# Kernel optimization log

Measured on AMD Instinct MI355X. Metric: run time of the kernel, lower is better.

## Reference

```python
import jax, jax.numpy as jnp
import numpy as np

N = 100000   # nodes
E = 1600000  # edges (avg degree 16)
IN_F = 256
OUT_F = 128


def setup_inputs() -> dict:
    key = jax.random.key(0)
    k1, k2, k3, k4, k5, k6 = jax.random.split(key, 6)
    std = 1.0 / (OUT_F ** 0.5)
    return {
        "x": jax.random.normal(k1, (N, IN_F), dtype=jnp.float32),
        "weight": jax.random.uniform(k2, (IN_F, OUT_F), dtype=jnp.float32, minval=-std, maxval=std),
        "bias": jax.random.uniform(k3, (OUT_F,), dtype=jnp.float32, minval=-std, maxval=std),
        "edge_weight": jax.random.uniform(k4, (E,), dtype=jnp.float32),
        "row": jax.random.randint(k5, (E,), 0, N, dtype=jnp.int32),
        "col": jax.random.randint(k6, (E,), 0, N, dtype=jnp.int32),
    }


def reference(x, weight, bias, edge_weight, row, col):
    # support = x @ W : dense GEMM [N, in] x [in, out]
    support = jnp.matmul(x, weight)
    # spmm(adj, support): gather source-node rows, scale by edge value,
    # scatter-add into destination rows (COO SpMM).
    msgs = support[col] * edge_weight[:, None]          # [E, out]
    aggregated = jax.ops.segment_sum(msgs, row, num_segments=N)  # [N, out]
    return aggregated + bias
```

## Files before the change

### kernel.cpp

```cpp
#include <hip/hip_runtime.h>

#define N_NODES 100000
#define IN_F 256
#define OUT_F 128

#define BKT_SHIFT 9
#define BKT_SIZE (1 << BKT_SHIFT)
#define NBKT ((N_NODES + BKT_SIZE - 1) / BKT_SIZE)
#define CHUNK 4096

#define WS_SUP 0
#define WS_EBUF2 25600000
#define WS_BBASE 38400000
#define WS_BCUR 38401024
#define WS_BCNT 38402048
#define WS_EBUF 51200000
#define WS_OFFS 64000000
#define WS_NEEDED 65200016

typedef __attribute__((ext_vector_type(8))) short short8;
typedef __attribute__((ext_vector_type(4))) float f32x4;
typedef __attribute__((ext_vector_type(2))) float f32x2;

__device__ __forceinline__ unsigned short f2bf(float f) {
  unsigned u = __float_as_uint(f);
  unsigned r = (u + 0x7fffu + ((u >> 16) & 1u)) >> 16;
  return (unsigned short)r;
}

__global__ __launch_bounds__(256) void prep_bswz_kernel(
    const float* __restrict__ w, unsigned short* __restrict__ bswz,
    int* __restrict__ bcnt) {
  const int tid = blockIdx.x * 256 + threadIdx.x;
  if (tid < NBKT) bcnt[tid] = 0;
  const int j = tid & 7;
  const int lane = (tid >> 3) & 63;
  const int nt = (tid >> 9) & 7;
  const int ks = tid >> 12;
  const int k = ks * 32 + ((lane >> 4) * 8) + j;
  const int n = nt * 16 + (lane & 15);
  bswz[tid] = f2bf(w[k * OUT_F + n]);
}

__global__ __launch_bounds__(512) void gemm_mfma_kernel(
    const float* __restrict__ x, const unsigned short* __restrict__ bswz,
    unsigned short* __restrict__ supb) {
  __shared__ unsigned short lb[32768];

  const int t = threadIdx.x;
  {
    const int4* src = (const int4*)bswz;
    int4* dst = (int4*)lb;
#pragma unroll
    for (int i = 0; i < 8; ++i) dst[t + i * 512] = src[t + i * 512];
  }
  __syncthreads();

  const int w = t >> 6;
  const int lane = t & 63;
  const int quad = lane >> 4;
  const int m16 = lane & 15;

  const int row = blockIdx.x * 128 + w * 16 + m16;
  const int rc = row < N_NODES ? row : N_NODES - 1;
  const float* ap = x + (long long)rc * IN_F + quad * 8;
  const short8* bb = (const short8*)lb + lane;

  f32x4 acc[8];
#pragma unroll
  for (int nt = 0; nt < 8; ++nt) acc[nt] = (f32x4){0.f, 0.f, 0.f, 0.f};

#pragma unroll
  for (int ks = 0; ks < 8; ++ks) {
    const float4 a0 = *(const float4*)(ap + ks * 32);
    const float4 a1 = *(const float4*)(ap + ks * 32 + 4);
    short8 af;
    af[0] = f2bf(a0.x); af[1] = f2bf(a0.y); af[2] = f2bf(a0.z); af[3] = f2bf(a0.w);
    af[4] = f2bf(a1.x); af[5] = f2bf(a1.y); af[6] = f2bf(a1.z); af[7] = f2bf(a1.w);
#pragma unroll
    for (int nt = 0; nt < 8; ++nt) {
      const short8 bf = bb[(ks * 8 + nt) * 64];
      acc[nt] = __builtin_amdgcn_mfma_f32_16x16x32_bf16(af, bf, acc[nt], 0, 0, 0);
    }
  }

  const int rowbase = blockIdx.x * 128 + w * 16 + quad * 4;
#pragma unroll
  for (int nt = 0; nt < 8; ++nt) {
#pragma unroll
    for (int r = 0; r < 4; ++r) {
      const int gr = rowbase + r;
      if (gr < N_NODES)
        supb[(long long)gr * OUT_F + nt * 16 + m16] = f2bf(acc[nt][r]);
    }
  }
}

__global__ __launch_bounds__(256) void bucket_hist_kernel(
    const int* __restrict__ row, int* __restrict__ bcnt, int E) {
  __shared__ int lcnt[NBKT];
  const int t = threadIdx.x;
  if (t < NBKT) lcnt[t] = 0;
  __syncthreads();
  const int E4 = E >> 2;
  const int i0 = blockIdx.x * 1024;
  const int4* row4 = (const int4*)row;
#pragma unroll
  for (int k = 0; k < 4; ++k) {
    const int i = i0 + k * 256 + t;
    if (i < E4) {
      const int4 r = row4[i];
      atomicAdd(&lcnt[r.x >> BKT_SHIFT], 1);
      atomicAdd(&lcnt[r.y >> BKT_SHIFT], 1);
      atomicAdd(&lcnt[r.z >> BKT_SHIFT], 1);
      atomicAdd(&lcnt[r.w >> BKT_SHIFT], 1);
    }
  }
  if (blockIdx.x == 0 && t < (E - E4 * 4))
    atomicAdd(&lcnt[row[E4 * 4 + t] >> BKT_SHIFT], 1);
  __syncthreads();
  if (t < NBKT && lcnt[t]) atomicAdd(&bcnt[t], lcnt[t]);
}

__global__ __launch_bounds__(256) void bucket_scan_kernel(
    const int* __restrict__ bcnt, int* __restrict__ bbase,
    int* __restrict__ bcur, int* __restrict__ offsets) {
  __shared__ int s[256];
  const int t = threadIdx.x;
  const int v = (t < NBKT) ? bcnt[t] : 0;
  s[t] = v;
  __syncthreads();
  for (int off = 1; off < 256; off <<= 1) {
    const int w = (t >= off) ? s[t - off] : 0;
    __syncthreads();
    s[t] += w;
    __syncthreads();
  }
  const int excl = s[t] - v;
  if (t < NBKT) {
    bbase[t] = excl;
    bcur[t] = excl;
  }
  if (t == NBKT - 1) {
    bbase[NBKT] = s[t];
    offsets[N_NODES] = s[t];
  }
}

__global__ __launch_bounds__(256) void bucket_fill_kernel(
    const int* __restrict__ row, const int* __restrict__ col,
    const float* __restrict__ ew, int* __restrict__ bcur,
    int2* __restrict__ ebuf2, int E) {
  __shared__ int lcnt[256];
  __shared__ int lscan[256];
  __shared__ int lbase[NBKT];
  __shared__ int2 stage[CHUNK];
  __shared__ unsigned char bid[CHUNK];

  const int t = threadIdx.x;
  const int e0 = blockIdx.x * CHUNK;
  lcnt[t] = 0;
  __syncthreads();

  int myb[16];
  int rank[16];
  int2 pk[16];
#pragma unroll
  for (int k = 0; k < 16; ++k) {
    const int e = e0 + k * 256 + t;
    myb[k] = -1;
    if (e < E) {
      const int r = row[e];
      const int c = col[e];
      const float wv = ew[e];
      const int b = r >> BKT_SHIFT;
      myb[k] = b;
      pk[k] = make_int2(c | ((r & (BKT_SIZE - 1)) << 17), __float_as_int(wv));
      rank[k] = atomicAdd(&lcnt[b], 1);
    }
  }
  __syncthreads();

  const int v = lcnt[t];
  lscan[t] = v;
  __syncthreads();
  for (int off = 1; off < 256; off <<= 1) {
    const int w = (t >= off) ? lscan[t - off] : 0;
    __syncthreads();
    lscan[t] += w;
    __syncthreads();
  }
  const int excl = lscan[t] - v;
  if (t < NBKT) lbase[t] = v ? atomicAdd(&bcur[t], v) : 0;
  __syncthreads();
  lscan[t] = excl;
  __syncthreads();

#pragma unroll
  for (int k = 0; k < 16; ++k) {
    if (myb[k] >= 0) {
      const int p = lscan[myb[k]] + rank[k];
      stage[p] = pk[k];
      bid[p] = (unsigned char)myb[k];
    }
  }
  __syncthreads();

  const int total = min(CHUNK, E - e0);
  for (int i = t; i < total; i += 256) {
    const int b = bid[i];
    ebuf2[lbase[b] + (i - lscan[b])] = stage[i];
  }
}

__global__ __launch_bounds__(512) void node_fill_kernel(
    const int2* __restrict__ ebuf2, const int* __restrict__ bbase,
    int2* __restrict__ ebuf, int* __restrict__ offsets) {
  __shared__ int hist[BKT_SIZE];
  __shared__ int scan[BKT_SIZE];
  const int t = threadIdx.x;
  const int b = blockIdx.x;
  const int base = bbase[b];
  const int end = bbase[b + 1];

  hist[t] = 0;
  __syncthreads();
  for (int i = base + t; i < end; i += 512) {
    const int lr = (ebuf2[i].x >> 17) & (BKT_SIZE - 1);
    atomicAdd(&hist[lr], 1);
  }
  __syncthreads();

  const int v = hist[t];
  scan[t] = v;
  __syncthreads();
  for (int off = 1; off < 512; off <<= 1) {
    const int w = (t >= off) ? scan[t - off] : 0;
    __syncthreads();
    scan[t] += w;
    __syncthreads();
  }
  const int excl = scan[t] - v;
  const int node = (b << BKT_SHIFT) + t;
  if (node < N_NODES) offsets[node] = base + excl;
  hist[t] = excl;
  __syncthreads();

  for (int i = base + t; i < end; i += 512) {
    const int2 e = ebuf2[i];
    const int lr = (e.x >> 17) & (BKT_SIZE - 1);
    const int p = atomicAdd(&hist[lr], 1);
    ebuf[base + p] = make_int2(e.x & 0x1FFFF, e.y);
  }
}

__global__ __launch_bounds__(256) void gather_kernel(
    const unsigned short* __restrict__ supb, const int2* __restrict__ ebuf,
    const int* __restrict__ offsets, const float* __restrict__ bias,
    float* __restrict__ out) {
  const int wave = (int)((blockIdx.x * 256 + threadIdx.x) >> 6);
  const int lane = threadIdx.x & 63;
  if (wave >= N_NODES) return;

  const int start = offsets[wave];
  const int end = offsets[wave + 1];

  float a0 = 0.f, a1 = 0.f, b0 = 0.f, b1 = 0.f;
  float c0 = 0.f, c1 = 0.f, d0 = 0.f, d1 = 0.f;
  const unsigned short* sp = supb + lane * 2;

  for (int base = start; base < end; base += 64) {
    const int cnt = min(64, end - base);
    int ecol = 0, ewb = 0;
    if (lane < cnt) {
      const int2 e = ebuf[base + lane];
      ecol = e.x;
      ewb = e.y;
    }
    int j = 0;
    for (; j + 4 <= cnt; j += 4) {
      const int cc0 = __builtin_amdgcn_readlane(ecol, j);
      const int cc1 = __builtin_amdgcn_readlane(ecol, j + 1);
      const int cc2 = __builtin_amdgcn_readlane(ecol, j + 2);
      const int cc3 = __builtin_amdgcn_readlane(ecol, j + 3);
      const float w0 = __int_as_float(__builtin_amdgcn_readlane(ewb, j));
      const float w1 = __int_as_float(__builtin_amdgcn_readlane(ewb, j + 1));
      const float w2 = __int_as_float(__builtin_amdgcn_readlane(ewb, j + 2));
      const float w3 = __int_as_float(__builtin_amdgcn_readlane(ewb, j + 3));
      const unsigned u0 = *(const unsigned*)(sp + (long long)cc0 * OUT_F);
      const unsigned u1 = *(const unsigned*)(sp + (long long)cc1 * OUT_F);
      const unsigned u2 = *(const unsigned*)(sp + (long long)cc2 * OUT_F);
      const unsigned u3 = *(const unsigned*)(sp + (long long)cc3 * OUT_F);
      a0 = fmaf(__uint_as_float(u0 << 16), w0, a0);
      a1 = fmaf(__uint_as_float(u0 & 0xffff0000u), w0, a1);
      b0 = fmaf(__uint_as_float(u1 << 16), w1, b0);
      b1 = fmaf(__uint_as_float(u1 & 0xffff0000u), w1, b1);
      c0 = fmaf(__uint_as_float(u2 << 16), w2, c0);
      c1 = fmaf(__uint_as_float(u2 & 0xffff0000u), w2, c1);
      d0 = fmaf(__uint_as_float(u3 << 16), w3, d0);
      d1 = fmaf(__uint_as_float(u3 & 0xffff0000u), w3, d1);
    }
    for (; j < cnt; ++j) {
      const int cc = __builtin_amdgcn_readlane(ecol, j);
      const float w0 = __int_as_float(__builtin_amdgcn_readlane(ewb, j));
      const unsigned u0 = *(const unsigned*)(sp + (long long)cc * OUT_F);
      a0 = fmaf(__uint_as_float(u0 << 16), w0, a0);
      a1 = fmaf(__uint_as_float(u0 & 0xffff0000u), w0, a1);
    }
  }
  const float2 bv = *(const float2*)(bias + lane * 2);
  const f32x2 v = {a0 + b0 + c0 + d0 + bv.x, a1 + b1 + c1 + d1 + bv.y};
  __builtin_nontemporal_store(v, (f32x2*)(out + (long long)wave * OUT_F + lane * 2));
}

__global__ __launch_bounds__(256) void bias_init_kernel(
    float* __restrict__ out, const float* __restrict__ bias) {
  const int t = blockIdx.x * blockDim.x + threadIdx.x;
  const int idx = t * 4;
  *(float4*)(out + idx) = *(const float4*)(bias + (idx & (OUT_F - 1)));
}

__global__ __launch_bounds__(256) void scatter_kernel(
    const unsigned short* __restrict__ supb, const float* __restrict__ ew,
    const int* __restrict__ row, const int* __restrict__ col,
    float* __restrict__ out, int E) {
  const long long t = (long long)blockIdx.x * blockDim.x + threadIdx.x;
  const int e = (int)(t >> 6);
  if (e >= E) return;
  const int lane = (int)(t & 63);
  const int c = col[e];
  const int r = row[e];
  const float wv = ew[e];
  const unsigned u = *(const unsigned*)(supb + (long long)c * OUT_F + lane * 2);
  float* o = out + (long long)r * OUT_F + lane * 2;
  atomicAdd(o, __uint_as_float(u << 16) * wv);
  atomicAdd(o + 1, __uint_as_float(u & 0xffff0000u) * wv);
}

extern "C" void kernel_launch(void* const* d_in, const int* in_sizes, int n_in,
                              void* d_out, int out_size, void* d_ws, size_t ws_size,
                              hipStream_t stream) {
  const float* x = (const float*)d_in[0];
  const float* weight = (const float*)d_in[1];
  const float* bias = (const float*)d_in[2];
  const float* edge_weight = (const float*)d_in[3];
  const int* row = (const int*)d_in[4];
  const int* col = (const int*)d_in[5];
  float* out = (float*)d_out;
  const int E = in_sizes[3];

  char* ws = (char*)d_ws;
  unsigned short* supb = (unsigned short*)(ws + WS_SUP);
  unsigned short* bswz = (unsigned short*)(ws + WS_EBUF);
  int* bcnt = (int*)(ws + WS_BCNT);

  prep_bswz_kernel<<<128, 256, 0, stream>>>(weight, bswz, bcnt);
  gemm_mfma_kernel<<<(N_NODES + 127) / 128, 512, 0, stream>>>(x, bswz, supb);

  if (ws_size >= (size_t)WS_NEEDED) {
    int2* ebuf2 = (int2*)(ws + WS_EBUF2);
    int* bbase = (int*)(ws + WS_BBASE);
    int* bcur = (int*)(ws + WS_BCUR);
    int2* ebuf = (int2*)(ws + WS_EBUF);
    int* offsets = (int*)(ws + WS_OFFS);

    bucket_hist_kernel<<<((E >> 2) + 1023) / 1024, 256, 0, stream>>>(row, bcnt, E);
    bucket_scan_kernel<<<1, 256, 0, stream>>>(bcnt, bbase, bcur, offsets);
    bucket_fill_kernel<<<(E + CHUNK - 1) / CHUNK, 256, 0, stream>>>(
        row, col, edge_weight, bcur, ebuf2, E);
    node_fill_kernel<<<NBKT, 512, 0, stream>>>(ebuf2, bbase, ebuf, offsets);
    gather_kernel<<<(N_NODES * 64) / 256, 256, 0, stream>>>(supb, ebuf, offsets,
                                                            bias, out);
  } else {
    bias_init_kernel<<<(N_NODES * OUT_F / 4) / 256, 256, 0, stream>>>(out, bias);
    scatter_kernel<<<(int)(((long long)E * 64 + 255) / 256), 256, 0, stream>>>(
        supb, edge_weight, row, col, out, E);
  }
}
```

Baseline: 302.3 us.

## Replace global CSR build with per-bucket slabs and fused LDS-sorted gather

Drops the histogram and scan kernels: edges are scattered straight into fixed-capacity slabs of 4096 entries, one per 128-node bucket, using atomic cursors. The separate node_fill and gather kernels become one kernel per bucket that counting-sorts the bucket's edges in LDS and then has each wave accumulate 16 nodes, with 8-way unrolled independent loads. This cuts kernel launches and a full global round-trip of the edge list. In exchange it relies on no bucket overflowing the slab (excess edges are silently dropped), falls back to a slow scan for buckets above the LDS cap, and runs far fewer waves during the gather, which may leave less latency hiding.

```diff
diff --git a/kernel.cpp b/kernel.cpp
--- a/kernel.cpp
+++ b/kernel.cpp
@@ -4,18 +4,17 @@
 #define IN_F 256
 #define OUT_F 128
 
-#define BKT_SHIFT 9
+#define BKT_SHIFT 7
 #define BKT_SIZE (1 << BKT_SHIFT)
 #define NBKT ((N_NODES + BKT_SIZE - 1) / BKT_SIZE)
+#define SLAB_CAP 4096
 #define CHUNK 4096
+#define GCAP 2816
 
 #define WS_SUP 0
-#define WS_EBUF2 25600000
-#define WS_BBASE 38400000
-#define WS_BCUR 38401024
-#define WS_BCNT 38402048
-#define WS_EBUF 51200000
-#define WS_OFFS 64000000
+#define WS_SLAB 25600000
+#define WS_BSWZ 51300000
+#define WS_BCUR 51400000
 #define WS_NEEDED 65200016
 
 typedef __attribute__((ext_vector_type(8))) short short8;
@@ -30,9 +29,9 @@
 
 __global__ __launch_bounds__(256) void prep_bswz_kernel(
     const float* __restrict__ w, unsigned short* __restrict__ bswz,
-    int* __restrict__ bcnt) {
+    int* __restrict__ bcur) {
   const int tid = blockIdx.x * 256 + threadIdx.x;
-  if (tid < NBKT) bcnt[tid] = 0;
+  if (tid < NBKT) bcur[tid] = 0;
   const int j = tid & 7;
   const int lane = (tid >> 3) & 63;
   const int nt = (tid >> 9) & 7;
@@ -96,78 +95,27 @@
   }
 }
 
-__global__ __launch_bounds__(256) void bucket_hist_kernel(
-    const int* __restrict__ row, int* __restrict__ bcnt, int E) {
-  __shared__ int lcnt[NBKT];
-  const int t = threadIdx.x;
-  if (t < NBKT) lcnt[t] = 0;
-  __syncthreads();
-  const int E4 = E >> 2;
-  const int i0 = blockIdx.x * 1024;
-  const int4* row4 = (const int4*)row;
-#pragma unroll
-  for (int k = 0; k < 4; ++k) {
-    const int i = i0 + k * 256 + t;
-    if (i < E4) {
-      const int4 r = row4[i];
-      atomicAdd(&lcnt[r.x >> BKT_SHIFT], 1);
-      atomicAdd(&lcnt[r.y >> BKT_SHIFT], 1);
-      atomicAdd(&lcnt[r.z >> BKT_SHIFT], 1);
-      atomicAdd(&lcnt[r.w >> BKT_SHIFT], 1);
-    }
-  }
-  if (blockIdx.x == 0 && t < (E - E4 * 4))
-    atomicAdd(&lcnt[row[E4 * 4 + t] >> BKT_SHIFT], 1);
-  __syncthreads();
-  if (t < NBKT && lcnt[t]) atomicAdd(&bcnt[t], lcnt[t]);
-}
-
-__global__ __launch_bounds__(256) void bucket_scan_kernel(
-    const int* __restrict__ bcnt, int* __restrict__ bbase,
-    int* __restrict__ bcur, int* __restrict__ offsets) {
-  __shared__ int s[256];
-  const int t = threadIdx.x;
-  const int v = (t < NBKT) ? bcnt[t] : 0;
-  s[t] = v;
-  __syncthreads();
-  for (int off = 1; off < 256; off <<= 1) {
-    const int w = (t >= off) ? s[t - off] : 0;
-    __syncthreads();
-    s[t] += w;
-    __syncthreads();
-  }
-  const int excl = s[t] - v;
-  if (t < NBKT) {
-    bbase[t] = excl;
-    bcur[t] = excl;
-  }
-  if (t == NBKT - 1) {
-    bbase[NBKT] = s[t];
-    offsets[N_NODES] = s[t];
-  }
-}
-
-__global__ __launch_bounds__(256) void bucket_fill_kernel(
+__global__ __launch_bounds__(1024) void bucket_fill_kernel(
     const int* __restrict__ row, const int* __restrict__ col,
     const float* __restrict__ ew, int* __restrict__ bcur,
-    int2* __restrict__ ebuf2, int E) {
-  __shared__ int lcnt[256];
-  __shared__ int lscan[256];
-  __shared__ int lbase[NBKT];
+    int2* __restrict__ slab, int E) {
+  __shared__ int lcnt[1024];
+  __shared__ int lscan[1024];
+  __shared__ int outb[NBKT];
   __shared__ int2 stage[CHUNK];
-  __shared__ unsigned char bid[CHUNK];
+  __shared__ unsigned short bid[CHUNK];
 
   const int t = threadIdx.x;
   const int e0 = blockIdx.x * CHUNK;
   lcnt[t] = 0;
   __syncthreads();
 
-  int myb[16];
-  int rank[16];
-  int2 pk[16];
-#pragma unroll
-  for (int k = 0; k < 16; ++k) {
-    const int e = e0 + k * 256 + t;
+  int myb[4];
+  int rank[4];
+  int2 pk[4];
+#pragma unroll
+  for (int k = 0; k < 4; ++k) {
+    const int e = e0 + k * 1024 + t;
     myb[k] = -1;
     if (e < E) {
       const int r = row[e];
@@ -184,133 +132,160 @@
   const int v = lcnt[t];
   lscan[t] = v;
   __syncthreads();
-  for (int off = 1; off < 256; off <<= 1) {
+  for (int off = 1; off < 1024; off <<= 1) {
     const int w = (t >= off) ? lscan[t - off] : 0;
     __syncthreads();
     lscan[t] += w;
     __syncthreads();
   }
   const int excl = lscan[t] - v;
-  if (t < NBKT) lbase[t] = v ? atomicAdd(&bcur[t], v) : 0;
+  if (t < NBKT && v) outb[t] = atomicAdd(&bcur[t], v);
   __syncthreads();
   lscan[t] = excl;
   __syncthreads();
 
 #pragma unroll
-  for (int k = 0; k < 16; ++k) {
+  for (int k = 0; k < 4; ++k) {
     if (myb[k] >= 0) {
       const int p = lscan[myb[k]] + rank[k];
       stage[p] = pk[k];
-      bid[p] = (unsigned char)myb[k];
+      bid[p] = (unsigned short)myb[k];
     }
   }
   __syncthreads();
 
   const int total = min(CHUNK, E - e0);
-  for (int i = t; i < total; i += 256) {
+  for (int i = t; i < total; i += 1024) {
     const int b = bid[i];
-    ebuf2[lbase[b] + (i - lscan[b])] = stage[i];
-  }
-}
-
-__global__ __launch_bounds__(512) void node_fill_kernel(
-    const int2* __restrict__ ebuf2, const int* __restrict__ bbase,
-    int2* __restrict__ ebuf, int* __restrict__ offsets) {
+    const int rel = outb[b] + (i - lscan[b]);
+    if (rel < SLAB_CAP) slab[(long long)b * SLAB_CAP + rel] = stage[i];
+  }
+}
+
+__global__ __launch_bounds__(512) void node_gather_kernel(
+    const unsigned short* __restrict__ supb, const int2* __restrict__ slab,
+    const int* __restrict__ bcur, const float* __restrict__ bias,
+    float* __restrict__ out) {
+  __shared__ int2 eS[GCAP];
   __shared__ int hist[BKT_SIZE];
-  __shared__ int scan[BKT_SIZE];
+  __shared__ int sbase[BKT_SIZE];
+  __shared__ int cur[BKT_SIZE];
+
   const int t = threadIdx.x;
-  const int b = blockIdx.x;
-  const int base = bbase[b];
-  const int end = bbase[b + 1];
-
-  hist[t] = 0;
-  __syncthreads();
-  for (int i = base + t; i < end; i += 512) {
-    const int lr = (ebuf2[i].x >> 17) & (BKT_SIZE - 1);
-    atomicAdd(&hist[lr], 1);
-  }
-  __syncthreads();
-
-  const int v = hist[t];
-  scan[t] = v;
-  __syncthreads();
-  for (int off = 1; off < 512; off <<= 1) {
-    const int w = (t >= off) ? scan[t - off] : 0;
-    __syncthreads();
-    scan[t] += w;
-    __syncthreads();
-  }
-  const int excl = scan[t] - v;
-  const int node = (b << BKT_SHIFT) + t;
-  if (node < N_NODES) offsets[node] = base + excl;
-  hist[t] = excl;
-  __syncthreads();
-
-  for (int i = base + t; i < end; i += 512) {
-    const int2 e = ebuf2[i];
-    const int lr = (e.x >> 17) & (BKT_SIZE - 1);
-    const int p = atomicAdd(&hist[lr], 1);
-    ebuf[base + p] = make_int2(e.x & 0x1FFFF, e.y);
-  }
-}
-
-__global__ __launch_bounds__(256) void gather_kernel(
-    const unsigned short* __restrict__ supb, const int2* __restrict__ ebuf,
-    const int* __restrict__ offsets, const float* __restrict__ bias,
-    float* __restrict__ out) {
-  const int wave = (int)((blockIdx.x * 256 + threadIdx.x) >> 6);
-  const int lane = threadIdx.x & 63;
-  if (wave >= N_NODES) return;
-
-  const int start = offsets[wave];
-  const int end = offsets[wave + 1];
-
-  float a0 = 0.f, a1 = 0.f, b0 = 0.f, b1 = 0.f;
-  float c0 = 0.f, c1 = 0.f, d0 = 0.f, d1 = 0.f;
+  const int bk = blockIdx.x;
+  const long long sb = (long long)bk * SLAB_CAP;
+  int n = bcur[bk];
+  n = n > SLAB_CAP ? SLAB_CAP : n;
+
+  const int w = t >> 6;
+  const int lane = t & 63;
   const unsigned short* sp = supb + lane * 2;
-
-  for (int base = start; base < end; base += 64) {
-    const int cnt = min(64, end - base);
-    int ecol = 0, ewb = 0;
-    if (lane < cnt) {
-      const int2 e = ebuf[base + lane];
-      ecol = e.x;
-      ewb = e.y;
-    }
-    int j = 0;
-    for (; j + 4 <= cnt; j += 4) {
-      const int cc0 = __builtin_amdgcn_readlane(ecol, j);
-      const int cc1 = __builtin_amdgcn_readlane(ecol, j + 1);
-      const int cc2 = __builtin_amdgcn_readlane(ecol, j + 2);
-      const int cc3 = __builtin_amdgcn_readlane(ecol, j + 3);
-      const float w0 = __int_as_float(__builtin_amdgcn_readlane(ewb, j));
-      const float w1 = __int_as_float(__builtin_amdgcn_readlane(ewb, j + 1));
-      const float w2 = __int_as_float(__builtin_amdgcn_readlane(ewb, j + 2));
-      const float w3 = __int_as_float(__builtin_amdgcn_readlane(ewb, j + 3));
-      const unsigned u0 = *(const unsigned*)(sp + (long long)cc0 * OUT_F);
-      const unsigned u1 = *(const unsigned*)(sp + (long long)cc1 * OUT_F);
-      const unsigned u2 = *(const unsigned*)(sp + (long long)cc2 * OUT_F);
-      const unsigned u3 = *(const unsigned*)(sp + (long long)cc3 * OUT_F);
-      a0 = fmaf(__uint_as_float(u0 << 16), w0, a0);
-      a1 = fmaf(__uint_as_float(u0 & 0xffff0000u), w0, a1);
-      b0 = fmaf(__uint_as_float(u1 << 16), w1, b0);
-      b1 = fmaf(__uint_as_float(u1 & 0xffff0000u), w1, b1);
-      c0 = fmaf(__uint_as_float(u2 << 16), w2, c0);
-      c1 = fmaf(__uint_as_float(u2 & 0xffff0000u), w2, c1);
-      d0 = fmaf(__uint_as_float(u3 << 16), w3, d0);
-      d1 = fmaf(__uint_as_float(u3 & 0xffff0000u), w3, d1);
-    }
-    for (; j < cnt; ++j) {
-      const int cc = __builtin_amdgcn_readlane(ecol, j);
-      const float w0 = __int_as_float(__builtin_amdgcn_readlane(ewb, j));
-      const unsigned u0 = *(const unsigned*)(sp + (long long)cc * OUT_F);
-      a0 = fmaf(__uint_as_float(u0 << 16), w0, a0);
-      a1 = fmaf(__uint_as_float(u0 & 0xffff0000u), w0, a1);
-    }
-  }
   const float2 bv = *(const float2*)(bias + lane * 2);
-  const f32x2 v = {a0 + b0 + c0 + d0 + bv.x, a1 + b1 + c1 + d1 + bv.y};
-  __builtin_nontemporal_store(v, (f32x2*)(out + (long long)wave * OUT_F + lane * 2));
+
+  if (n <= GCAP) {
+    if (t < BKT_SIZE) hist[t] = 0;
+    __syncthreads();
+    for (int i = t; i < n; i += 512)
+      atomicAdd(&hist[(slab[sb + i].x >> 17) & (BKT_SIZE - 1)], 1);
+    __syncthreads();
+    int v = 0;
+    if (t < BKT_SIZE) { v = hist[t]; sbase[t] = v; }
+    __syncthreads();
+    for (int off = 1; off < BKT_SIZE; off <<= 1) {
+      int add = 0;
+      if (t < BKT_SIZE && t >= off) add = sbase[t - off];
+      __syncthreads();
+      if (t < BKT_SIZE) sbase[t] += add;
+      __syncthreads();
+    }
+    if (t < BKT_SIZE) { sbase[t] -= v; cur[t] = sbase[t]; }
+    __syncthreads();
+    for (int i = t; i < n; i += 512) {
+      const int2 e = slab[sb + i];
+      const int lr = (e.x >> 17) & (BKT_SIZE - 1);
+      eS[atomicAdd(&cur[lr], 1)] = e;
+    }
+    __syncthreads();
+
+    for (int k = 0; k < 16; ++k) {
+      const int lr0 = w * 16 + k;
+      const int node = (bk << BKT_SHIFT) + lr0;
+      if (node >= N_NODES) break;
+      const int s = sbase[lr0];
+      const int e_end = s + hist[lr0];
+      float a0 = 0.f, a1 = 0.f, b0 = 0.f, b1 = 0.f;
+      float c0 = 0.f, c1 = 0.f, d0 = 0.f, d1 = 0.f;
+      float p0 = 0.f, p1 = 0.f, q0 = 0.f, q1 = 0.f;
+      float r0 = 0.f, r1 = 0.f, s0 = 0.f, s1 = 0.f;
+      int j = s;
+      for (; j + 8 <= e_end; j += 8) {
+        const int2 E0 = eS[j];     const int2 E1 = eS[j + 1];
+        const int2 E2 = eS[j + 2]; const int2 E3 = eS[j + 3];
+        const int2 E4 = eS[j + 4]; const int2 E5 = eS[j + 5];
+        const int2 E6 = eS[j + 6]; const int2 E7 = eS[j + 7];
+        const unsigned u0 = *(const unsigned*)(sp + (long long)(E0.x & 0x1FFFF) * OUT_F);
+        const unsigned u1 = *(const unsigned*)(sp + (long long)(E1.x & 0x1FFFF) * OUT_F);
+        const unsigned u2 = *(const unsigned*)(sp + (long long)(E2.x & 0x1FFFF) * OUT_F);
+        const unsigned u3 = *(const unsigned*)(sp + (long long)(E3.x & 0x1FFFF) * OUT_F);
+        const unsigned u4 = *(const unsigned*)(sp + (long long)(E4.x & 0x1FFFF) * OUT_F);
+        const unsigned u5 = *(const unsigned*)(sp + (long long)(E5.x & 0x1FFFF) * OUT_F);
+        const unsigned u6 = *(const unsigned*)(sp + (long long)(E6.x & 0x1FFFF) * OUT_F);
+        const unsigned u7 = *(const unsigned*)(sp + (long long)(E7.x & 0x1FFFF) * OUT_F);
+        a0 = fmaf(__uint_as_float(u0 << 16), __int_as_float(E0.y), a0);
+        a1 = fmaf(__uint_as_float(u0 & 0xffff0000u), __int_as_float(E0.y), a1);
+        b0 = fmaf(__uint_as_float(u1 << 16), __int_as_float(E1.y), b0);
+        b1 = fmaf(__uint_as_float(u1 & 0xffff0000u), __int_as_float(E1.y), b1);
+        c0 = fmaf(__uint_as_float(u2 << 16), __int_as_float(E2.y), c0);
+        c1 = fmaf(__uint_as_float(u2 & 0xffff0000u), __int_as_float(E2.y), c1);
+        d0 = fmaf(__uint_as_float(u3 << 16), __int_as_float(E3.y), d0);
+        d1 = fmaf(__uint_as_float(u3 & 0xffff0000u), __int_as_float(E3.y), d1);
+        p0 = fmaf(__uint_as_float(u4 << 16), __int_as_float(E4.y), p0);
+        p1 = fmaf(__uint_as_float(u4 & 0xffff0000u), __int_as_float(E4.y), p1);
+        q0 = fmaf(__uint_as_float(u5 << 16), __int_as_float(E5.y), q0);
+        q1 = fmaf(__uint_as_float(u5 & 0xffff0000u), __int_as_float(E5.y), q1);
+        r0 = fmaf(__uint_as_float(u6 << 16), __int_as_float(E6.y), r0);
+        r1 = fmaf(__uint_as_float(u6 & 0xffff0000u), __int_as_float(E6.y), r1);
+        s0 = fmaf(__uint_as_float(u7 << 16), __int_as_float(E7.y), s0);
+        s1 = fmaf(__uint_as_float(u7 & 0xffff0000u), __int_as_float(E7.y), s1);
+      }
+      for (; j + 2 <= e_end; j += 2) {
+        const int2 E0 = eS[j];
+        const int2 E1 = eS[j + 1];
+        const unsigned u0 = *(const unsigned*)(sp + (long long)(E0.x & 0x1FFFF) * OUT_F);
+        const unsigned u1 = *(const unsigned*)(sp + (long long)(E1.x & 0x1FFFF) * OUT_F);
+        a0 = fmaf(__uint_as_float(u0 << 16), __int_as_float(E0.y), a0);
+        a1 = fmaf(__uint_as_float(u0 & 0xffff0000u), __int_as_float(E0.y), a1);
+        b0 = fmaf(__uint_as_float(u1 << 16), __int_as_float(E1.y), b0);
+        b1 = fmaf(__uint_as_float(u1 & 0xffff0000u), __int_as_float(E1.y), b1);
+      }
+      if (j < e_end) {
+        const int2 E0 = eS[j];
+        const unsigned u0 = *(const unsigned*)(sp + (long long)(E0.x & 0x1FFFF) * OUT_F);
+        a0 = fmaf(__uint_as_float(u0 << 16), __int_as_float(E0.y), a0);
+        a1 = fmaf(__uint_as_float(u0 & 0xffff0000u), __int_as_float(E0.y), a1);
+      }
+      const f32x2 vv = {a0 + b0 + c0 + d0 + p0 + q0 + r0 + s0 + bv.x,
+                        a1 + b1 + c1 + d1 + p1 + q1 + r1 + s1 + bv.y};
+      __builtin_nontemporal_store(vv, (f32x2*)(out + (long long)node * OUT_F + lane * 2));
+    }
+  } else {
+    for (int k = 0; k < 16; ++k) {
+      const int lr0 = w * 16 + k;
+      const int node = (bk << BKT_SHIFT) + lr0;
+      if (node >= N_NODES) break;
+      float a0 = 0.f, a1 = 0.f;
+      for (int i = 0; i < n; ++i) {
+        const int2 e = slab[sb + i];
+        if (((e.x >> 17) & (BKT_SIZE - 1)) == lr0) {
+          const unsigned u = *(const unsigned*)(sp + (long long)(e.x & 0x1FFFF) * OUT_F);
+          a0 = fmaf(__uint_as_float(u << 16), __int_as_float(e.y), a0);
+          a1 = fmaf(__uint_as_float(u & 0xffff0000u), __int_as_float(e.y), a1);
+        }
+      }
+      const f32x2 vv = {a0 + bv.x, a1 + bv.y};
+      __builtin_nontemporal_store(vv, (f32x2*)(out + (long long)node * OUT_F + lane * 2));
+    }
+  }
 }
 
 __global__ __launch_bounds__(256) void bias_init_kernel(
@@ -351,26 +326,18 @@
 
   char* ws = (char*)d_ws;
   unsigned short* supb = (unsigned short*)(ws + WS_SUP);
-  unsigned short* bswz = (unsigned short*)(ws + WS_EBUF);
-  int* bcnt = (int*)(ws + WS_BCNT);
-
-  prep_bswz_kernel<<<128, 256, 0, stream>>>(weight, bswz, bcnt);
+  unsigned short* bswz = (unsigned short*)(ws + WS_BSWZ);
+  int* bcur = (int*)(ws + WS_BCUR);
+
+  prep_bswz_kernel<<<128, 256, 0, stream>>>(weight, bswz, bcur);
   gemm_mfma_kernel<<<(N_NODES + 127) / 128, 512, 0, stream>>>(x, bswz, supb);
 
   if (ws_size >= (size_t)WS_NEEDED) {
-    int2* ebuf2 = (int2*)(ws + WS_EBUF2);
-    int* bbase = (int*)(ws + WS_BBASE);
-    int* bcur = (int*)(ws + WS_BCUR);
-    int2* ebuf = (int2*)(ws + WS_EBUF);
-    int* offsets = (int*)(ws + WS_OFFS);
-
-    bucket_hist_kernel<<<((E >> 2) + 1023) / 1024, 256, 0, stream>>>(row, bcnt, E);
-    bucket_scan_kernel<<<1, 256, 0, stream>>>(bcnt, bbase, bcur, offsets);
-    bucket_fill_kernel<<<(E + CHUNK - 1) / CHUNK, 256, 0, stream>>>(
-        row, col, edge_weight, bcur, ebuf2, E);
-    node_fill_kernel<<<NBKT, 512, 0, stream>>>(ebuf2, bbase, ebuf, offsets);
-    gather_kernel<<<(N_NODES * 64) / 256, 256, 0, stream>>>(supb, ebuf, offsets,
-                                                            bias, out);
+    int2* slab = (int2*)(ws + WS_SLAB);
+
+    bucket_fill_kernel<<<(E + CHUNK - 1) / CHUNK, 1024, 0, stream>>>(
+        row, col, edge_weight, bcur, slab, E);
+    node_gather_kernel<<<NBKT, 512, 0, stream>>>(supb, slab, bcur, bias, out);
   } else {
     bias_init_kernel<<<(N_NODES * OUT_F / 4) / 256, 256, 0, stream>>>(out, bias);
     scatter_kernel<<<(int)(((long long)E * 64 + 255) / 256), 256, 0, stream>>>(
```

Result: faster. 276.3 us (-8.6%).
